# Kernel tuning notes

Measured on AMD Instinct MI355X. Metric: run time of the kernel, lower is better.

Reference implementation:

```python
import jax, jax.numpy as jnp
import numpy as np
import itertools

WS = (4, 4, 4, 2, 2)          # window size per dim
SS = (2, 2, 2, 1, 1)          # shift size per dim
B, D, H, W, U, V, C = 1, 16, 16, 8, 8, 8, 128
HEADS = 4
HD = C // HEADS
N = WS[0] * WS[1] * WS[2] * WS[3] * WS[4]   # 256 tokens per window


def _partition(x):
    # (b, D,H,W,U,V, c) -> (b*nW, N, c)
    b, c = x.shape[0], x.shape[-1]
    x = x.reshape(b, D // WS[0], WS[0], H // WS[1], WS[1], W // WS[2], WS[2],
                  U // WS[3], WS[3], V // WS[4], WS[4], c)
    x = x.transpose(0, 1, 3, 5, 7, 9, 2, 4, 6, 8, 10, 11)
    return x.reshape(-1, N, c)


def _reverse(win, b):
    # (b*nW, N, c) -> (b, D,H,W,U,V, c)
    c = win.shape[-1]
    x = win.reshape(b, D // WS[0], H // WS[1], W // WS[2], U // WS[3], V // WS[4],
                    WS[0], WS[1], WS[2], WS[3], WS[4], c)
    x = x.transpose(0, 1, 6, 2, 7, 3, 8, 4, 9, 5, 10, 11)
    return x.reshape(b, D, H, W, U, V, c)


def _ln(x, w, b, eps=1e-5):
    mu = jnp.mean(x, -1, keepdims=True)
    xc = x - mu
    var = jnp.mean(xc * xc, -1, keepdims=True)
    return xc * jax.lax.rsqrt(var + eps) * w + b


def _compute_mask():
    # 5D generalization of Swin's compute_mask: region labels then pairwise diff
    img = np.zeros((1, D, H, W, U, V, 1), np.float32)
    slcs = [[slice(0, -w), slice(-w, -s), slice(-s, None)] for w, s in zip(WS, SS)]
    cnt = 0
    for idx in itertools.product(*slcs):
        img[(slice(None),) + idx] = cnt
        cnt += 1
    mw = np.asarray(_partition(jnp.asarray(img))).squeeze(-1)  # (nW, N)
    diff = mw[:, None, :] - mw[:, :, None]
    return jnp.asarray(np.where(diff != 0, -1e9, 0.0).astype(np.float32))


def setup_inputs() -> dict:
    key = jax.random.key(0)
    ks = jax.random.split(key, 6)
    s = 0.02
    return {
        "x": jax.random.normal(ks[0], (B, D, H, W, U, V, C), jnp.float32),
        "mask": _compute_mask(),  # (512, 256, 256)
        "qkv_w": jax.random.normal(ks[1], (3 * C, C), jnp.float32) * s,
        "qkv_b": jnp.zeros((3 * C,), jnp.float32),
        "proj_w": jax.random.normal(ks[2], (C, C), jnp.float32) * s,
        "proj_b": jnp.zeros((C,), jnp.float32),
        "norm1_w": jnp.ones((C,), jnp.float32),
        "norm1_b": jnp.zeros((C,), jnp.float32),
        "norm2_w": jnp.ones((C,), jnp.float32),
        "norm2_b": jnp.zeros((C,), jnp.float32),
        "fc1_w": jax.random.normal(ks[3], (4 * C, C), jnp.float32) * s,
        "fc1_b": jnp.zeros((4 * C,), jnp.float32),
        "fc2_w": jax.random.normal(ks[4], (C, 4 * C), jnp.float32) * s,
        "fc2_b": jnp.zeros((C,), jnp.float32),
    }


def reference(x, mask, qkv_w, qkv_b, proj_w, proj_b, norm1_w, norm1_b,
              norm2_w, norm2_b, fc1_w, fc1_b, fc2_w, fc2_b):
    shortcut = x
    h = _ln(x, norm1_w, norm1_b)
    # cyclic shift
    h = jnp.roll(h, shift=tuple(-s for s in SS), axis=(1, 2, 3, 4, 5))
    win = _partition(h)                                # (nW, N, C)
    nw = win.shape[0]
    qkv = win @ qkv_w.T + qkv_b                        # (nW, N, 3C)
    qkv = qkv.reshape(nw, N, 3, HEADS, HD).transpose(2, 0, 3, 1, 4)
    q, k, v = qkv[0] * (HD ** -0.5), qkv[1], qkv[2]    # (nW, heads, N, hd)
    logits = jnp.einsum('bhnc,bhmc->bhnm', q, k) + mask[:, None]
    attn = jax.nn.softmax(logits, axis=-1)
    o = jnp.einsum('bhnm,bhmc->bhnc', attn, v)
    o = o.transpose(0, 2, 1, 3).reshape(nw, N, C)
    o = o @ proj_w.T + proj_b
    h = _reverse(o, B)
    # reverse cyclic shift
    h = jnp.roll(h, shift=SS, axis=(1, 2, 3, 4, 5))
    x = shortcut + h
    m = _ln(x, norm2_w, norm2_b)
    m = jax.nn.gelu(m @ fc1_w.T + fc1_b, approximate=False)
    m = m @ fc2_w.T + fc2_b
    return x + m
```

## Files before the change

kernel.cpp:

```cpp
#include <hip/hip_runtime.h>
#include <math.h>

typedef short bf16x8 __attribute__((ext_vector_type(8)));
typedef float f32x4 __attribute__((ext_vector_type(4)));
typedef unsigned short ushort_t;
typedef unsigned int uint_t;

__device__ __forceinline__ float bf2f(ushort_t h) { return __uint_as_float(((uint_t)h) << 16); }
__device__ __forceinline__ ushort_t f2bf(float f) {
    uint_t u = __float_as_uint(f);
    u += 0x7fffu + ((u >> 16) & 1u);
    return (ushort_t)(u >> 16);
}
__device__ __forceinline__ float bflo(uint_t u) { return __uint_as_float(u << 16); }
__device__ __forceinline__ float bfhi(uint_t u) { return __uint_as_float(u & 0xffff0000u); }

__device__ __forceinline__ bool probe_f32(const void* ones) {
    return ((const ushort_t*)ones)[0] == 0;
}

__device__ __forceinline__ void load8f(const void* p, size_t idx, bool f32, float* o) {
    if (f32) {
        const float4* q = (const float4*)((const float*)p + idx);
        float4 a = q[0], b = q[1];
        o[0] = a.x; o[1] = a.y; o[2] = a.z; o[3] = a.w;
        o[4] = b.x; o[5] = b.y; o[6] = b.z; o[7] = b.w;
    } else {
        uint4 u = *(const uint4*)((const ushort_t*)p + idx);
        o[0] = bflo(u.x); o[1] = bfhi(u.x); o[2] = bflo(u.y); o[3] = bfhi(u.y);
        o[4] = bflo(u.z); o[5] = bfhi(u.z); o[6] = bflo(u.w); o[7] = bfhi(u.w);
    }
}

__device__ __forceinline__ float load1(const void* p, size_t i, bool f32) {
    return f32 ? ((const float*)p)[i] : bf2f(((const ushort_t*)p)[i]);
}
__device__ __forceinline__ void store1(void* p, size_t i, bool f32, float v) {
    if (f32) ((float*)p)[i] = v;
    else ((ushort_t*)p)[i] = f2bf(v);
}

__device__ __forceinline__ float gelu_f(float x) {
    float ax = fabsf(x) * 0.70710678118654752f;
    float t = __builtin_amdgcn_rcpf(1.f + 0.3275911f * ax);
    float p = t * (0.254829592f +
              t * (-0.284496736f +
              t * (1.421413741f +
              t * (-1.453152027f +
              t * 1.061405429f))));
    float e = __expf(-ax * ax);
    float erfv = 1.f - p * e;
    float phi = 0.5f * (1.f + copysignf(erfv, x));
    return x * phi;
}

__device__ __forceinline__ void token_g(int t, int g[5]) {
    int n = t & 255, w = t >> 8;
    int wv = w & 3, wu = (w >> 2) & 3, ww = (w >> 4) & 1, wh = (w >> 5) & 3, wd = (w >> 7) & 3;
    int iv = n & 1, iu = (n >> 1) & 1, iw = (n >> 2) & 3, ih = (n >> 4) & 3, id = (n >> 6) & 3;
    g[0] = wd * 4 + id;
    g[1] = wh * 4 + ih;
    g[2] = ww * 4 + iw;
    g[3] = wu * 2 + iu;
    g[4] = wv * 2 + iv;
}

__device__ __forceinline__ int token_shiftpix(int t) {
    int g[5];
    token_g(t, g);
    int d = (g[0] + 2) & 15, h = (g[1] + 2) & 15, w = (g[2] + 2) & 7;
    int u = (g[3] + 1) & 7, v = (g[4] + 1) & 7;
    return ((((d * 16 + h) * 8 + w) * 8 + u) * 8 + v);
}

__device__ __forceinline__ int token_label(int t) {
    int g[5];
    token_g(t, g);
    int r0 = g[0] < 12 ? 0 : (g[0] < 14 ? 1 : 2);
    int r1 = g[1] < 12 ? 0 : (g[1] < 14 ? 1 : 2);
    int r2 = g[2] < 4 ? 0 : (g[2] < 6 ? 1 : 2);
    int r3 = g[3] < 6 ? 0 : (g[3] < 7 ? 1 : 2);
    int r4 = g[4] < 6 ? 0 : (g[4] < 7 ? 1 : 2);
    return (((r0 * 3 + r1) * 3 + r2) * 3 + r3) * 3 + r4;
}

#define MFMA16(a, b, c) __builtin_amdgcn_mfma_f32_16x16x32_bf16(a, b, c, 0, 0, 0)

#define QW_N 49152
#define PW_N 16384
#define W1_N 65536
#define W2_N 65536

__global__ __launch_bounds__(256) void k_prep(const void* __restrict__ qw,
                                              const void* __restrict__ pw,
                                              const void* __restrict__ w1,
                                              const void* __restrict__ w2,
                                              const void* __restrict__ probe,
                                              ushort_t* __restrict__ out) {
    const bool f32 = probe_f32(probe);
    size_t e = ((size_t)blockIdx.x * 256 + threadIdx.x) * 8;
    float v[8];
    size_t dst;
    if (e < QW_N) {
        load8f(qw, e, f32, v);
        int n = (int)(e >> 7), k = (int)(e & 127);
        int chunk = ((n >> 4) * 4 + (k >> 5)) * 64 + ((k >> 3) & 3) * 16 + (n & 15);
        dst = (size_t)chunk * 8;
    } else if (e < QW_N + PW_N) {
        size_t off = e - QW_N;
        load8f(pw, off, f32, v);
        int n = (int)(off >> 7), k = (int)(off & 127);
        int chunk = ((n >> 4) * 4 + (k >> 5)) * 64 + ((k >> 3) & 3) * 16 + (n & 15);
        dst = (size_t)QW_N + (size_t)chunk * 8;
    } else if (e < QW_N + PW_N + W1_N) {
        size_t off = e - (QW_N + PW_N);
        load8f(w1, off, f32, v);
        int n = (int)(off >> 7), k = (int)(off & 127);
        int chunk = ((n >> 4) * 4 + (k >> 5)) * 64 + ((k >> 3) & 3) * 16 + (n & 15);
        dst = (size_t)(QW_N + PW_N) + (size_t)chunk * 8;
    } else {
        size_t off = e - (QW_N + PW_N + W1_N);
        load8f(w2, off, f32, v);
        int n = (int)(off >> 9), k = (int)(off & 511);
        int chunk = ((n >> 4) * 16 + (k >> 5)) * 64 + ((k >> 3) & 3) * 16 + (n & 15);
        dst = (size_t)(QW_N + PW_N + W1_N) + (size_t)chunk * 8;
    }
    union { uint4 q; ushort_t u[8]; } pk;
#pragma unroll
    for (int j = 0; j < 8; j++) pk.u[j] = f2bf(v[j]);
    *reinterpret_cast<uint4*>(out + dst) = pk.q;
}

__global__ __launch_bounds__(256) void k_qkv(const void* __restrict__ x,
                                             const void* __restrict__ n1w,
                                             const void* __restrict__ n1b,
                                             const ushort_t* __restrict__ qwF,
                                             const void* __restrict__ qb,
                                             ushort_t* __restrict__ qT,
                                             ushort_t* __restrict__ kT,
                                             ushort_t* __restrict__ vF) {
    __shared__ __align__(16) ushort_t sA[64][136];
    const bool f32 = probe_f32(n1w);
    const int tid = threadIdx.x;
    const int rt = blockIdx.x;

    {
        int i = tid >> 2, q4 = tid & 3;
        int t = rt * 64 + i;
        int pix = token_shiftpix(t);
        float v[32];
        float s1 = 0.f, s2 = 0.f;
#pragma unroll
        for (int j = 0; j < 4; j++) {
            load8f(x, (size_t)pix * 128 + q4 * 32 + j * 8, f32, &v[j * 8]);
#pragma unroll
            for (int e = 0; e < 8; e++) { float f = v[j * 8 + e]; s1 += f; s2 += f * f; }
        }
        s1 += __shfl_xor(s1, 1);
        s2 += __shfl_xor(s2, 1);
        s1 += __shfl_xor(s1, 2);
        s2 += __shfl_xor(s2, 2);
        float mean = s1 * (1.f / 128.f);
        float var = s2 * (1.f / 128.f) - mean * mean;
        float rstd = rsqrtf(fmaxf(var, 0.f) + 1e-5f);
#pragma unroll
        for (int j = 0; j < 4; j++) {
            float wv[8], bv[8];
            load8f(n1w, q4 * 32 + j * 8, f32, wv);
            load8f(n1b, q4 * 32 + j * 8, f32, bv);
            union { uint4 q; ushort_t u[8]; } pk;
#pragma unroll
            for (int e = 0; e < 8; e++)
                pk.u[e] = f2bf((v[j * 8 + e] - mean) * rstd * wv[e] + bv[e]);
            *reinterpret_cast<uint4*>(&sA[i][q4 * 32 + j * 8]) = pk.q;
        }
    }
    __syncthreads();

    const int lane = tid & 63, wvid = tid >> 6, quad = lane >> 4, l16 = lane & 15;
    const int wbase4 = (rt >> 2) * 4;
    const int nadd = (rt & 3) * 64;

#pragma unroll 1
    for (int ct = 0; ct < 3; ct++) {
        f32x4 acc[4][2];
#pragma unroll
        for (int a = 0; a < 4; a++)
#pragma unroll
            for (int b = 0; b < 2; b++) acc[a][b] = (f32x4){0.f, 0.f, 0.f, 0.f};

#pragma unroll 2
        for (int k4 = 0; k4 < 4; k4++) {
            bf16x8 af[4], bg[2];
#pragma unroll
            for (int mi = 0; mi < 4; mi++)
                af[mi] = *reinterpret_cast<const bf16x8*>(&sA[mi * 16 + l16][k4 * 32 + quad * 8]);
#pragma unroll
            for (int ni = 0; ni < 2; ni++)
                bg[ni] = *reinterpret_cast<const bf16x8*>(
                    qwF + (size_t)(((ct * 8 + wvid * 2 + ni) * 4 + k4) * 64 + lane) * 8);
#pragma unroll
            for (int mi = 0; mi < 4; mi++)
#pragma unroll
                for (int ni = 0; ni < 2; ni++) acc[mi][ni] = MFMA16(af[mi], bg[ni], acc[mi][ni]);
        }
#pragma unroll
        for (int ni = 0; ni < 2; ni++) {
            int col = wvid * 32 + ni * 16 + l16;
            float bias = load1(qb, ct * 128 + col, f32);
            int h = col >> 5, d = col & 31;
            size_t whbase = (size_t)(wbase4 + h) * 8192;
#pragma unroll
            for (int mi = 0; mi < 4; mi++) {
#pragma unroll
                for (int r = 0; r < 4; r++) {
                    int row = mi * 16 + quad * 4 + r;
                    int n = nadd + row;
                    float val = acc[mi][ni][r] + bias;
                    if (ct == 0) {
                        qT[whbase + (size_t)n * 32 + d] = f2bf(val);
                    } else if (ct == 1) {
                        kT[whbase + (size_t)n * 32 + d] = f2bf(val);
                    } else {
                        size_t idx = whbase + (size_t)(n >> 5) * 1024 + (size_t)(d >> 4) * 512 +
                                     (size_t)((n >> 3) & 3) * 128 + (size_t)(d & 15) * 8 + (n & 7);
                        vF[idx] = f2bf(val);
                    }
                }
            }
        }
    }
}

__global__ __launch_bounds__(256) void k_attn(const ushort_t* __restrict__ qT,
                                              const ushort_t* __restrict__ kT,
                                              const ushort_t* __restrict__ vF,
                                              ushort_t* __restrict__ o) {
    __shared__ __align__(16) ushort_t sS[64][264];
    __shared__ unsigned char sLab[256];
    const int tid = threadIdx.x;
    const int hh = blockIdx.x, w = blockIdx.y;
    const size_t whbase = (size_t)(w * 4 + hh) * 8192;

    sLab[tid] = (unsigned char)token_label(w * 256 + tid);
    __syncthreads();

    const int lane = tid & 63, wvid = tid >> 6, quad = lane >> 4, l16 = lane & 15;
    const int r0 = wvid * 16;

#pragma unroll 1
    for (int rb = 0; rb < 4; rb++) {
        bf16x8 aq = *reinterpret_cast<const bf16x8*>(
            qT + whbase + (size_t)(rb * 64 + r0 + l16) * 32 + quad * 8);

        f32x4 s[16];
        int myLab[4];
#pragma unroll
        for (int r = 0; r < 4; r++) myLab[r] = sLab[rb * 64 + r0 + quad * 4 + r];
#pragma unroll
        for (int ni = 0; ni < 16; ni++) {
            bf16x8 bk = *reinterpret_cast<const bf16x8*>(
                kT + whbase + (size_t)(ni * 16 + l16) * 32 + quad * 8);
            f32x4 c = (f32x4){0.f, 0.f, 0.f, 0.f};
            c = MFMA16(aq, bk, c);
            int klab = sLab[ni * 16 + l16];
#pragma unroll
            for (int r = 0; r < 4; r++)
                s[ni][r] = (klab == myLab[r]) ? c[r] * 0.17677669529663687f : -1.0e30f;
        }
        float mx[4], sm[4], inv[4];
#pragma unroll
        for (int r = 0; r < 4; r++) {
            float m2 = s[0][r];
#pragma unroll
            for (int ni = 1; ni < 16; ni++) m2 = fmaxf(m2, s[ni][r]);
            m2 = fmaxf(m2, __shfl_xor(m2, 1));
            m2 = fmaxf(m2, __shfl_xor(m2, 2));
            m2 = fmaxf(m2, __shfl_xor(m2, 4));
            m2 = fmaxf(m2, __shfl_xor(m2, 8));
            mx[r] = m2;
        }
#pragma unroll
        for (int r = 0; r < 4; r++) sm[r] = 0.f;
#pragma unroll
        for (int ni = 0; ni < 16; ni++) {
#pragma unroll
            for (int r = 0; r < 4; r++) {
                float p = __expf(s[ni][r] - mx[r]);
                s[ni][r] = p;
                sm[r] += p;
            }
        }
#pragma unroll
        for (int r = 0; r < 4; r++) {
            float t2 = sm[r];
            t2 += __shfl_xor(t2, 1);
            t2 += __shfl_xor(t2, 2);
            t2 += __shfl_xor(t2, 4);
            t2 += __shfl_xor(t2, 8);
            inv[r] = 1.f / t2;
        }
#pragma unroll
        for (int ni = 0; ni < 16; ni++) {
#pragma unroll
            for (int r = 0; r < 4; r++)
                sS[r0 + quad * 4 + r][ni * 16 + l16] = f2bf(s[ni][r]);
        }

        f32x4 oacc[2];
        oacc[0] = (f32x4){0.f, 0.f, 0.f, 0.f};
        oacc[1] = (f32x4){0.f, 0.f, 0.f, 0.f};
#pragma unroll
        for (int kt = 0; kt < 8; kt++) {
            bf16x8 ap = *reinterpret_cast<const bf16x8*>(&sS[r0 + l16][kt * 32 + quad * 8]);
#pragma unroll
            for (int t2 = 0; t2 < 2; t2++) {
                bf16x8 bv = *reinterpret_cast<const bf16x8*>(
                    vF + whbase + (size_t)((kt * 2 + t2) * 64 + lane) * 8);
                oacc[t2] = MFMA16(ap, bv, oacc[t2]);
            }
        }
#pragma unroll
        for (int t2 = 0; t2 < 2; t2++) {
#pragma unroll
            for (int r = 0; r < 4; r++) {
                int row = r0 + quad * 4 + r;
                int tok = w * 256 + rb * 64 + row;
                o[(size_t)tok * 128 + hh * 32 + t2 * 16 + l16] = f2bf(oacc[t2][r] * inv[r]);
            }
        }
    }
}

__global__ __launch_bounds__(256) void k_proj(const ushort_t* __restrict__ o,
                                              const ushort_t* __restrict__ pwF,
                                              const void* __restrict__ pb,
                                              const void* __restrict__ x,
                                              const void* __restrict__ n1w,
                                              float* __restrict__ x2) {
    __shared__ __align__(16) ushort_t sA[64][136];
    __shared__ int sPix[64];
    const bool f32 = probe_f32(n1w);
    const int tid = threadIdx.x;
    const int rt = blockIdx.x;

    if (tid < 64) sPix[tid] = token_shiftpix(rt * 64 + tid);
    {
        int i = tid >> 2, q4 = tid & 3;
        const uint4* src = (const uint4*)(o + (size_t)(rt * 64 + i) * 128 + q4 * 32);
#pragma unroll
        for (int j = 0; j < 4; j++)
            *reinterpret_cast<uint4*>(&sA[i][q4 * 32 + j * 8]) = src[j];
    }
    __syncthreads();

    const int lane = tid & 63, wvid = tid >> 6;
    const int quad = lane >> 4, l16 = lane & 15;
    f32x4 acc[4][2];
#pragma unroll
    for (int a = 0; a < 4; a++)
#pragma unroll
        for (int b = 0; b < 2; b++) acc[a][b] = (f32x4){0.f, 0.f, 0.f, 0.f};

#pragma unroll 2
    for (int k4 = 0; k4 < 4; k4++) {
        bf16x8 af[4], bg[2];
#pragma unroll
        for (int mi = 0; mi < 4; mi++)
            af[mi] = *reinterpret_cast<const bf16x8*>(&sA[mi * 16 + l16][k4 * 32 + quad * 8]);
#pragma unroll
        for (int ni = 0; ni < 2; ni++)
            bg[ni] = *reinterpret_cast<const bf16x8*>(
                pwF + (size_t)(((wvid * 2 + ni) * 4 + k4) * 64 + lane) * 8);
#pragma unroll
        for (int mi = 0; mi < 4; mi++)
#pragma unroll
            for (int ni = 0; ni < 2; ni++) acc[mi][ni] = MFMA16(af[mi], bg[ni], acc[mi][ni]);
    }
#pragma unroll
    for (int ni = 0; ni < 2; ni++) {
        int col = wvid * 32 + ni * 16 + l16;
        float bias = load1(pb, col, f32);
#pragma unroll
        for (int mi = 0; mi < 4; mi++) {
#pragma unroll
            for (int r = 0; r < 4; r++) {
                int row = mi * 16 + quad * 4 + r;
                int pix = sPix[row];
                size_t idx = (size_t)pix * 128 + col;
                x2[idx] = acc[mi][ni][r] + bias + load1(x, idx, f32);
            }
        }
    }
}

__global__ __launch_bounds__(256) void k_mlp(const float* __restrict__ x2,
                                             const void* __restrict__ n2w,
                                             const void* __restrict__ n2b,
                                             const ushort_t* __restrict__ w1f,
                                             const void* __restrict__ b1,
                                             const ushort_t* __restrict__ w2f,
                                             const void* __restrict__ b2,
                                             void* __restrict__ out) {
    __shared__ __align__(16) ushort_t sH[32][512];
    ushort_t (*sM)[136] = reinterpret_cast<ushort_t (*)[136]>(&sH[0][0]);
    const bool f32 = probe_f32(n2w);
    const int tid = threadIdx.x;
    const int t0 = blockIdx.x * 32;

    {
        int i = tid >> 3, oct = tid & 7;
        const float* row = x2 + (size_t)(t0 + i) * 128 + oct * 16;
        float v[16];
        float s1 = 0.f, s2 = 0.f;
#pragma unroll
        for (int j = 0; j < 4; j++) {
            float4 f = ((const float4*)row)[j];
            v[j * 4 + 0] = f.x; v[j * 4 + 1] = f.y; v[j * 4 + 2] = f.z; v[j * 4 + 3] = f.w;
            s1 += f.x + f.y + f.z + f.w;
            s2 += f.x * f.x + f.y * f.y + f.z * f.z + f.w * f.w;
        }
        s1 += __shfl_xor(s1, 1); s2 += __shfl_xor(s2, 1);
        s1 += __shfl_xor(s1, 2); s2 += __shfl_xor(s2, 2);
        s1 += __shfl_xor(s1, 4); s2 += __shfl_xor(s2, 4);
        float mean = s1 * (1.f / 128.f);
        float rstd = rsqrtf(fmaxf(s2 * (1.f / 128.f) - mean * mean, 0.f) + 1e-5f);
#pragma unroll
        for (int j = 0; j < 16; j++) {
            int c = oct * 16 + j;
            sM[i][c] = f2bf((v[j] - mean) * rstd * load1(n2w, c, f32) + load1(n2b, c, f32));
        }
    }
    __syncthreads();

    const int lane = tid & 63, wvid = tid >> 6, quad = lane >> 4, l16 = lane & 15;

    bf16x8 af[2][4];
#pragma unroll
    for (int mi = 0; mi < 2; mi++)
#pragma unroll
        for (int k4 = 0; k4 < 4; k4++)
            af[mi][k4] = *reinterpret_cast<const bf16x8*>(&sM[mi * 16 + l16][k4 * 32 + quad * 8]);
    __syncthreads();

    {
        const int cb = wvid * 128;
        bf16x8 wf[4], wn[4];
#pragma unroll
        for (int k4 = 0; k4 < 4; k4++)
            wf[k4] = *reinterpret_cast<const bf16x8*>(
                w1f + (size_t)(((wvid * 8) * 4 + k4) * 64 + lane) * 8);
#pragma unroll
        for (int ni = 0; ni < 8; ni++) {
            if (ni < 7) {
#pragma unroll
                for (int k4 = 0; k4 < 4; k4++)
                    wn[k4] = *reinterpret_cast<const bf16x8*>(
                        w1f + (size_t)(((wvid * 8 + ni + 1) * 4 + k4) * 64 + lane) * 8);
            }
            f32x4 a0 = (f32x4){0.f, 0.f, 0.f, 0.f};
            f32x4 a1 = (f32x4){0.f, 0.f, 0.f, 0.f};
#pragma unroll
            for (int k4 = 0; k4 < 4; k4++) {
                a0 = MFMA16(af[0][k4], wf[k4], a0);
                a1 = MFMA16(af[1][k4], wf[k4], a1);
            }
            int col = cb + ni * 16 + l16;
            int chunk = col >> 3, cl = col & 7;
            float bias = load1(b1, col, f32);
#pragma unroll
            for (int r = 0; r < 4; r++) {
                int row = quad * 4 + r;
                int swc = ((chunk ^ (row & 7)) << 3) | cl;
                sH[row][swc] = f2bf(gelu_f(a0[r] + bias));
                sH[16 + row][swc] = f2bf(gelu_f(a1[r] + bias));
            }
#pragma unroll
            for (int k4 = 0; k4 < 4; k4++) wf[k4] = wn[k4];
        }
    }
    __syncthreads();
    {
        const int cb = wvid * 32;
        float res[2][2][4];
#pragma unroll
        for (int mi = 0; mi < 2; mi++)
#pragma unroll
            for (int ni = 0; ni < 2; ni++)
#pragma unroll
                for (int r = 0; r < 4; r++)
                    res[mi][ni][r] = x2[(size_t)(t0 + mi * 16 + quad * 4 + r) * 128 + cb + ni * 16 + l16];
        f32x4 acc[2][2];
#pragma unroll
        for (int mi = 0; mi < 2; mi++)
#pragma unroll
            for (int ni = 0; ni < 2; ni++) acc[mi][ni] = (f32x4){0.f, 0.f, 0.f, 0.f};
        bf16x8 wf[2], wn[2];
#pragma unroll
        for (int ni = 0; ni < 2; ni++)
            wf[ni] = *reinterpret_cast<const bf16x8*>(
                w2f + (size_t)(((wvid * 2 + ni) * 16) * 64 + lane) * 8);
#pragma unroll
        for (int k0 = 0; k0 < 16; k0++) {
            if (k0 < 15) {
#pragma unroll
                for (int ni = 0; ni < 2; ni++)
                    wn[ni] = *reinterpret_cast<const bf16x8*>(
                        w2f + (size_t)(((wvid * 2 + ni) * 16 + k0 + 1) * 64 + lane) * 8);
            }
            int rc = ((k0 * 4 + quad) ^ (l16 & 7)) << 3;
            bf16x8 a0 = *reinterpret_cast<const bf16x8*>(&sH[l16][rc]);
            bf16x8 a1 = *reinterpret_cast<const bf16x8*>(&sH[16 + l16][rc]);
            acc[0][0] = MFMA16(a0, wf[0], acc[0][0]);
            acc[1][0] = MFMA16(a1, wf[0], acc[1][0]);
            acc[0][1] = MFMA16(a0, wf[1], acc[0][1]);
            acc[1][1] = MFMA16(a1, wf[1], acc[1][1]);
            wf[0] = wn[0];
            wf[1] = wn[1];
        }
#pragma unroll
        for (int ni = 0; ni < 2; ni++) {
            int col = cb + ni * 16 + l16;
            float bias = load1(b2, col, f32);
#pragma unroll
            for (int mi = 0; mi < 2; mi++) {
#pragma unroll
                for (int r = 0; r < 4; r++) {
                    int row = mi * 16 + quad * 4 + r;
                    size_t idx = (size_t)(t0 + row) * 128 + col;
                    store1(out, idx, f32, acc[mi][ni][r] + bias + res[mi][ni][r]);
                }
            }
        }
    }
}

extern "C" void kernel_launch(void* const* d_in, const int* in_sizes, int n_in,
                              void* d_out, int out_size, void* d_ws, size_t ws_size,
                              hipStream_t stream) {
    (void)in_sizes; (void)n_in; (void)out_size; (void)ws_size;
    const void* x   = d_in[0];
    const void* qw  = d_in[2];
    const void* qb  = d_in[3];
    const void* pw  = d_in[4];
    const void* pb  = d_in[5];
    const void* n1w = d_in[6];
    const void* n1b = d_in[7];
    const void* n2w = d_in[8];
    const void* n2b = d_in[9];
    const void* w1  = d_in[10];
    const void* b1  = d_in[11];
    const void* w2  = d_in[12];
    const void* b2  = d_in[13];

    ushort_t* qT  = (ushort_t*)d_ws;
    ushort_t* kT  = (ushort_t*)((char*)d_ws + 33554432);
    ushort_t* vF  = (ushort_t*)((char*)d_ws + 67108864);
    ushort_t* ob  = (ushort_t*)((char*)d_ws + 100663296);
    float* x2     = (float*)d_ws;
    ushort_t* wts = (ushort_t*)((char*)d_ws + 134217728);
    ushort_t* qwF = wts;
    ushort_t* pwF = wts + QW_N;
    ushort_t* w1f = wts + QW_N + PW_N;
    ushort_t* w2f = wts + QW_N + PW_N + W1_N;

    hipLaunchKernelGGL(k_prep, dim3(96), dim3(256), 0, stream, qw, pw, w1, w2, n1w, wts);
    hipLaunchKernelGGL(k_qkv, dim3(2048), dim3(256), 0, stream, x, n1w, n1b, qwF, qb, qT, kT, vF);
    hipLaunchKernelGGL(k_attn, dim3(4, 512), dim3(256), 0, stream, qT, kT, vF, ob);
    hipLaunchKernelGGL(k_proj, dim3(2048), dim3(256), 0, stream, ob, pwF, pb, x, n1w, x2);
    hipLaunchKernelGGL(k_mlp, dim3(4096), dim3(256), 0, stream, x2, n2w, n2b, w1f, b1, w2f, b2, d_out);
}
```

Before: 507.2 us.

## Double MLP row tile to 64 tokens with 8 waves per block

The fused MLP kernel now handles 64 tokens per block with 512 threads instead of 32 tokens with 256 threads. Each wave computes a narrower output column slice across four 16-row subtiles, so every weight fragment loaded from global memory feeds more MFMAs. The LDS swizzle gains an extra XOR term per row group to limit bank conflicts. The cost is double the shared memory (64 KB) and more registers per thread, which may reduce occupancy.

```diff
diff --git a/kernel.cpp b/kernel.cpp
--- a/kernel.cpp
+++ b/kernel.cpp
@@ -394,7 +394,7 @@
     }
 }
 
-__global__ __launch_bounds__(256) void k_mlp(const float* __restrict__ x2,
+__global__ __launch_bounds__(512) void k_mlp(const float* __restrict__ x2,
                                              const void* __restrict__ n2w,
                                              const void* __restrict__ n2b,
                                              const ushort_t* __restrict__ w1f,
@@ -402,11 +402,11 @@
                                              const ushort_t* __restrict__ w2f,
                                              const void* __restrict__ b2,
                                              void* __restrict__ out) {
-    __shared__ __align__(16) ushort_t sH[32][512];
+    __shared__ __align__(16) ushort_t sH[64][512];
     ushort_t (*sM)[136] = reinterpret_cast<ushort_t (*)[136]>(&sH[0][0]);
     const bool f32 = probe_f32(n2w);
     const int tid = threadIdx.x;
-    const int t0 = blockIdx.x * 32;
+    const int t0 = blockIdx.x * 64;
 
     {
         int i = tid >> 3, oct = tid & 7;
@@ -435,45 +435,49 @@
 
     const int lane = tid & 63, wvid = tid >> 6, quad = lane >> 4, l16 = lane & 15;
 
-    bf16x8 af[2][4];
-#pragma unroll
-    for (int mi = 0; mi < 2; mi++)
+    bf16x8 af[4][4];
+#pragma unroll
+    for (int s = 0; s < 4; s++)
 #pragma unroll
         for (int k4 = 0; k4 < 4; k4++)
-            af[mi][k4] = *reinterpret_cast<const bf16x8*>(&sM[mi * 16 + l16][k4 * 32 + quad * 8]);
+            af[s][k4] = *reinterpret_cast<const bf16x8*>(&sM[s * 16 + l16][k4 * 32 + quad * 8]);
     __syncthreads();
 
     {
-        const int cb = wvid * 128;
+        const int cb = wvid * 64;
         bf16x8 wf[4], wn[4];
 #pragma unroll
         for (int k4 = 0; k4 < 4; k4++)
             wf[k4] = *reinterpret_cast<const bf16x8*>(
-                w1f + (size_t)(((wvid * 8) * 4 + k4) * 64 + lane) * 8);
-#pragma unroll
-        for (int ni = 0; ni < 8; ni++) {
-            if (ni < 7) {
+                w1f + (size_t)(((wvid * 4) * 4 + k4) * 64 + lane) * 8);
+#pragma unroll
+        for (int ni = 0; ni < 4; ni++) {
+            if (ni < 3) {
 #pragma unroll
                 for (int k4 = 0; k4 < 4; k4++)
                     wn[k4] = *reinterpret_cast<const bf16x8*>(
-                        w1f + (size_t)(((wvid * 8 + ni + 1) * 4 + k4) * 64 + lane) * 8);
-            }
-            f32x4 a0 = (f32x4){0.f, 0.f, 0.f, 0.f};
-            f32x4 a1 = (f32x4){0.f, 0.f, 0.f, 0.f};
+                        w1f + (size_t)(((wvid * 4 + ni + 1) * 4 + k4) * 64 + lane) * 8);
+            }
+            f32x4 a[4];
+#pragma unroll
+            for (int s = 0; s < 4; s++) a[s] = (f32x4){0.f, 0.f, 0.f, 0.f};
 #pragma unroll
             for (int k4 = 0; k4 < 4; k4++) {
-                a0 = MFMA16(af[0][k4], wf[k4], a0);
-                a1 = MFMA16(af[1][k4], wf[k4], a1);
+#pragma unroll
+                for (int s = 0; s < 4; s++)
+                    a[s] = MFMA16(af[s][k4], wf[k4], a[s]);
             }
             int col = cb + ni * 16 + l16;
             int chunk = col >> 3, cl = col & 7;
             float bias = load1(b1, col, f32);
 #pragma unroll
-            for (int r = 0; r < 4; r++) {
-                int row = quad * 4 + r;
-                int swc = ((chunk ^ (row & 7)) << 3) | cl;
-                sH[row][swc] = f2bf(gelu_f(a0[r] + bias));
-                sH[16 + row][swc] = f2bf(gelu_f(a1[r] + bias));
+            for (int s = 0; s < 4; s++) {
+#pragma unroll
+                for (int r = 0; r < 4; r++) {
+                    int row = s * 16 + quad * 4 + r;
+                    int swc = ((chunk ^ (row & 7) ^ ((row >> 4) << 1)) << 3) | cl;
+                    sH[row][swc] = f2bf(gelu_f(a[s][r] + bias));
+                }
             }
 #pragma unroll
             for (int k4 = 0; k4 < 4; k4++) wf[k4] = wn[k4];
@@ -481,55 +485,41 @@
     }
     __syncthreads();
     {
-        const int cb = wvid * 32;
-        float res[2][2][4];
-#pragma unroll
-        for (int mi = 0; mi < 2; mi++)
-#pragma unroll
-            for (int ni = 0; ni < 2; ni++)
-#pragma unroll
-                for (int r = 0; r < 4; r++)
-                    res[mi][ni][r] = x2[(size_t)(t0 + mi * 16 + quad * 4 + r) * 128 + cb + ni * 16 + l16];
-        f32x4 acc[2][2];
-#pragma unroll
-        for (int mi = 0; mi < 2; mi++)
-#pragma unroll
-            for (int ni = 0; ni < 2; ni++) acc[mi][ni] = (f32x4){0.f, 0.f, 0.f, 0.f};
-        bf16x8 wf[2], wn[2];
-#pragma unroll
-        for (int ni = 0; ni < 2; ni++)
-            wf[ni] = *reinterpret_cast<const bf16x8*>(
-                w2f + (size_t)(((wvid * 2 + ni) * 16) * 64 + lane) * 8);
+        const int cb = wvid * 16;
+        float res[4][4];
+#pragma unroll
+        for (int s = 0; s < 4; s++)
+#pragma unroll
+            for (int r = 0; r < 4; r++)
+                res[s][r] = x2[(size_t)(t0 + s * 16 + quad * 4 + r) * 128 + cb + l16];
+        f32x4 acc[4];
+#pragma unroll
+        for (int s = 0; s < 4; s++) acc[s] = (f32x4){0.f, 0.f, 0.f, 0.f};
+        bf16x8 wf2, wn2;
+        wf2 = *reinterpret_cast<const bf16x8*>(
+            w2f + (size_t)((wvid * 16) * 64 + lane) * 8);
 #pragma unroll
         for (int k0 = 0; k0 < 16; k0++) {
             if (k0 < 15) {
-#pragma unroll
-                for (int ni = 0; ni < 2; ni++)
-                    wn[ni] = *reinterpret_cast<const bf16x8*>(
-                        w2f + (size_t)(((wvid * 2 + ni) * 16 + k0 + 1) * 64 + lane) * 8);
-            }
-            int rc = ((k0 * 4 + quad) ^ (l16 & 7)) << 3;
-            bf16x8 a0 = *reinterpret_cast<const bf16x8*>(&sH[l16][rc]);
-            bf16x8 a1 = *reinterpret_cast<const bf16x8*>(&sH[16 + l16][rc]);
-            acc[0][0] = MFMA16(a0, wf[0], acc[0][0]);
-            acc[1][0] = MFMA16(a1, wf[0], acc[1][0]);
-            acc[0][1] = MFMA16(a0, wf[1], acc[0][1]);
-            acc[1][1] = MFMA16(a1, wf[1], acc[1][1]);
-            wf[0] = wn[0];
-            wf[1] = wn[1];
-        }
-#pragma unroll
-        for (int ni = 0; ni < 2; ni++) {
-            int col = cb + ni * 16 + l16;
-            float bias = load1(b2, col, f32);
-#pragma unroll
-            for (int mi = 0; mi < 2; mi++) {
-#pragma unroll
-                for (int r = 0; r < 4; r++) {
-                    int row = mi * 16 + quad * 4 + r;
-                    size_t idx = (size_t)(t0 + row) * 128 + col;
-                    store1(out, idx, f32, acc[mi][ni][r] + bias + res[mi][ni][r]);
-                }
+                wn2 = *reinterpret_cast<const bf16x8*>(
+                    w2f + (size_t)((wvid * 16 + k0 + 1) * 64 + lane) * 8);
+            }
+#pragma unroll
+            for (int s = 0; s < 4; s++) {
+                int rc = ((k0 * 4 + quad) ^ (l16 & 7) ^ (s << 1)) << 3;
+                bf16x8 h = *reinterpret_cast<const bf16x8*>(&sH[s * 16 + l16][rc]);
+                acc[s] = MFMA16(h, wf2, acc[s]);
+            }
+            wf2 = wn2;
+        }
+        int col = cb + l16;
+        float bias = load1(b2, col, f32);
+#pragma unroll
+        for (int s = 0; s < 4; s++) {
+#pragma unroll
+            for (int r = 0; r < 4; r++) {
+                size_t idx = (size_t)(t0 + s * 16 + quad * 4 + r) * 128 + col;
+                store1(out, idx, f32, acc[s][r] + bias + res[s][r]);
             }
         }
     }
@@ -568,5 +558,5 @@
     hipLaunchKernelGGL(k_qkv, dim3(2048), dim3(256), 0, stream, x, n1w, n1b, qwF, qb, qT, kT, vF);
     hipLaunchKernelGGL(k_attn, dim3(4, 512), dim3(256), 0, stream, qT, kT, vF, ob);
     hipLaunchKernelGGL(k_proj, dim3(2048), dim3(256), 0, stream, ob, pwF, pb, x, n1w, x2);
-    hipLaunchKernelGGL(k_mlp, dim3(4096), dim3(256), 0, stream, x2, n2w, n2b, w1f, b1, w2f, b2, d_out);
-}
+    hipLaunchKernelGGL(k_mlp, dim3(2048), dim3(512), 0, stream, x2, n2w, n2b, w1f, b1, w2f, b2, d_out);
+}
```

New measurement: 540.6 us. 1.07x slower.
